# Performance work log

Measured on AMD Instinct MI355X. Metric: run time of the kernel, lower is better.

Reference implementation:

```python
import jax, jax.numpy as jnp
import numpy as np

N_NODES = 50000
N_EDGES = 800000
EDGE_DIM = 16
EMB = 128
BN_EPS = 1e-5


def setup_inputs() -> dict:
    key = jax.random.key(0)
    ks = jax.random.split(key, 8)
    node_feats = jax.random.normal(ks[0], (N_NODES, EMB), jnp.float32)
    edge_feats = jax.random.normal(ks[1], (N_EDGES, EDGE_DIM), jnp.float32)
    src = jax.random.randint(ks[2], (N_EDGES,), 0, N_NODES, dtype=jnp.int32)
    dst = jax.random.randint(ks[3], (N_EDGES,), 0, N_NODES, dtype=jnp.int32)
    def kaiming(k, shape, fan_in):
        return (jax.random.normal(k, shape, jnp.float32) / np.float32(np.sqrt(fan_in)))
    W_edge = kaiming(ks[4], (EDGE_DIM, EMB), EDGE_DIM)
    b_edge = jnp.zeros((EMB,), jnp.float32)
    W1 = kaiming(ks[5], (EMB, 2 * EMB), EMB)
    b1 = jnp.zeros((2 * EMB,), jnp.float32)
    W2 = kaiming(ks[6], (2 * EMB, EMB), 2 * EMB)
    b2 = jnp.zeros((EMB,), jnp.float32)
    bn_gamma = jnp.ones((EMB,), jnp.float32)
    bn_beta = jnp.zeros((EMB,), jnp.float32)
    return dict(node_feats=node_feats, edge_feats=edge_feats, W_edge=W_edge,
                b_edge=b_edge, W1=W1, b1=b1, W2=W2, b2=b2,
                bn_gamma=bn_gamma, bn_beta=bn_beta, src=src, dst=dst)


def reference(node_feats, edge_feats, W_edge, b_edge, W1, b1, W2, b2,
              bn_gamma, bn_beta, src, dst):
    n_nodes = node_feats.shape[0]
    # edge embedding: Linear(num_edge_emb -> emb_dim)
    edge_embeds = edge_feats @ W_edge + b_edge            # [E, D]
    # u_add_e message: gather source node feats, add edge embeds
    msg = node_feats[src] + edge_embeds                   # [E, D]
    # sum aggregation to destination nodes
    agg = jax.ops.segment_sum(msg, dst, num_segments=n_nodes)  # [N, D]
    # MLP: Linear(D, 2D) -> ReLU -> Linear(2D, D)
    h = jax.nn.relu(agg @ W1 + b1) @ W2 + b2              # [N, D]
    # BatchNorm1d over the node (batch) dim, training-mode batch stats
    mean = jnp.mean(h, axis=0)
    var = jnp.mean((h - mean) ** 2, axis=0)               # biased variance
    out = (h - mean) * jax.lax.rsqrt(var + BN_EPS) * bn_gamma + bn_beta
    return out
```

## Files before the change

kernel.cpp:

```cpp
#include <hip/hip_runtime.h>
#include <stdint.h>

#define NN 50000
#define NE 800000
#define CAP 128
#define NB_MLP ((NN + 63) / 64)

typedef unsigned int u32;
typedef unsigned short u16;
typedef __attribute__((ext_vector_type(8))) short short8;
typedef __attribute__((ext_vector_type(4))) float f32x4;
typedef int int4u __attribute__((ext_vector_type(4), aligned(4)));

__device__ __align__(16) u16   g_nf16[NN * 128];
__device__ __align__(16) u16   g_agg16[NN * 128];
__device__ __align__(16) float g_h[NN * 128];
__device__ __align__(16) float g_We[16 * 128];
__device__ __align__(16) float g_be[128];
__device__ __align__(16) float g_b1[256];
__device__ __align__(16) float g_b2[128];
__device__ __align__(16) float g_gamma[128];
__device__ __align__(16) float g_beta[128];
__device__ __align__(16) u16   g_W1p[128 * 256];
__device__ __align__(16) u16   g_W2p[256 * 128];
__device__ __align__(16) int2  g_bkt[NN * CAP];

__device__ __align__(16) int   g_zero[NN + 256];
#define g_cursor (g_zero)
#define g_stats  ((float*)(g_zero + NN))

__device__ __forceinline__ float bf2f(u16 u) {
  return __uint_as_float(((u32)u) << 16);
}
__device__ __forceinline__ u16 f2bf(float x) {
  u32 u = __float_as_uint(x);
  u32 r = (u + 0x7fffu + ((u >> 16) & 1u)) >> 16;
  return (u16)r;
}
__device__ __forceinline__ bool is_bf16(const u32* probe) {
  return probe[0] == 0x3F803F80u;
}

__global__ void k_prep(const void* nodep,
                       const void* We, const void* be, const void* W1,
                       const void* b1, const void* W2, const void* b2,
                       const void* ga, const void* bt, const u32* probe) {
  const bool b16 = is_bf16(probe);
  const int gid = blockIdx.x * blockDim.x + threadIdx.x;
  const int stride = gridDim.x * blockDim.x;
  if (!b16) {
    const float2* s = (const float2*)nodep;
    u32* d = (u32*)g_nf16;
    for (int i = gid; i < NN * 64; i += stride) {
      float2 v = s[i];
      d[i] = (u32)f2bf(v.x) | ((u32)f2bf(v.y) << 16);
    }
  }
  const int i = gid;
  if (i < 2816) {
    const void* s; float* d; int off;
    if      (i < 2048) { s = We; d = g_We;    off = i; }
    else if (i < 2176) { s = be; d = g_be;    off = i - 2048; }
    else if (i < 2432) { s = b1; d = g_b1;    off = i - 2176; }
    else if (i < 2560) { s = b2; d = g_b2;    off = i - 2432; }
    else if (i < 2688) { s = ga; d = g_gamma; off = i - 2560; }
    else               { s = bt; d = g_beta;  off = i - 2688; }
    d[off] = b16 ? bf2f(((const u16*)s)[off]) : ((const float*)s)[off];
  } else if (i < 35584) {
    const int idx = i - 2816;
    const int j = idx & 7, lane = (idx >> 3) & 63, nt = (idx >> 9) & 15, kt = idx >> 13;
    const int k = kt * 32 + (lane >> 4) * 8 + j;
    const int n = nt * 16 + (lane & 15);
    g_W1p[idx] = b16 ? ((const u16*)W1)[k * 256 + n]
                     : f2bf(((const float*)W1)[k * 256 + n]);
  } else if (i < 68352) {
    const int idx = i - 35584;
    const int j = idx & 7, lane = (idx >> 3) & 63, nt = (idx >> 9) & 7, kt = idx >> 12;
    const int k = kt * 32 + (lane >> 4) * 8 + j;
    const int n = nt * 16 + (lane & 15);
    g_W2p[idx] = b16 ? ((const u16*)W2)[k * 128 + n]
                     : f2bf(((const float*)W2)[k * 128 + n]);
  }
}

__global__ __launch_bounds__(256) void scatter_kernel(const int* __restrict__ src,
                                                      const int* __restrict__ dst, int E) {
  const int e = blockIdx.x * blockDim.x + threadIdx.x;
  if (e >= E) return;
  const int d = dst[e];
  const int c = atomicAdd(&g_cursor[d], 1);
  if (c < CAP) g_bkt[d * CAP + c] = make_int2(e, src[e]);
}

__device__ __forceinline__ void accum8(float* acc, uint4 v) {
  const u32 vv[4] = {v.x, v.y, v.z, v.w};
#pragma unroll
  for (int q = 0; q < 4; ++q) {
    acc[2 * q]     += bf2f((u16)vv[q]);
    acc[2 * q + 1] += bf2f((u16)(vv[q] >> 16));
  }
}
template <bool B16>
__device__ __forceinline__ float ef_at(const void* efin, size_t idx) {
  if constexpr (B16) return bf2f(((const u16*)efin)[idx]);
  else               return ((const float*)efin)[idx];
}
template <bool B16>
__device__ __forceinline__ void agg_body(const u16* __restrict__ nf,
                                         const void* __restrict__ efin) {
  const int tid  = threadIdx.x;
  const int wv   = tid >> 6;
  const int lane = tid & 63;
  const int g    = lane >> 4;
  const int i16  = lane & 15;
  const int t    = blockIdx.x * 4 + wv;
  if (t >= NN) return;
  const int degc = g_cursor[t];
  const int deg  = degc < CAP ? degc : CAP;
  const int base = t * CAP;
  const int d0 = i16 * 8;

  const int q4 = deg >> 2, r4 = deg & 3;
  const int gs = g * q4 + (g < r4 ? g : r4);
  const int ge = gs + q4 + (g < r4 ? 1 : 0);

  float acc[8];
#pragma unroll
  for (int q = 0; q < 8; ++q) acc[q] = 0.f;
  float sEF = 0.f;

  int jj = gs;
  for (; jj + 3 < ge; jj += 4) {
    const int* ep = (const int*)g_bkt + 2 * (base + jj);
    int4u ea = *(const int4u*)ep;
    int4u eb = *(const int4u*)(ep + 4);
    uint4 v0 = *(const uint4*)(nf + (size_t)ea.y * 128 + d0);
    uint4 v1 = *(const uint4*)(nf + (size_t)ea.w * 128 + d0);
    uint4 v2 = *(const uint4*)(nf + (size_t)eb.y * 128 + d0);
    uint4 v3 = *(const uint4*)(nf + (size_t)eb.w * 128 + d0);
    float f0 = ef_at<B16>(efin, (size_t)ea.x * 16 + i16);
    float f1 = ef_at<B16>(efin, (size_t)ea.z * 16 + i16);
    float f2 = ef_at<B16>(efin, (size_t)eb.x * 16 + i16);
    float f3 = ef_at<B16>(efin, (size_t)eb.z * 16 + i16);
    accum8(acc, v0);
    accum8(acc, v1);
    accum8(acc, v2);
    accum8(acc, v3);
    sEF += (f0 + f1) + (f2 + f3);
  }
  const int rem = ge - jj;
  if (rem > 0) {
    int2 p0 = g_bkt[base + jj];
    int2 p1 = (rem > 1) ? g_bkt[base + jj + 1] : p0;
    int2 p2 = (rem > 2) ? g_bkt[base + jj + 2] : p0;
    uint4 v0 = *(const uint4*)(nf + (size_t)p0.y * 128 + d0);
    uint4 v1 = *(const uint4*)(nf + (size_t)p1.y * 128 + d0);
    uint4 v2 = *(const uint4*)(nf + (size_t)p2.y * 128 + d0);
    float f0 = ef_at<B16>(efin, (size_t)p0.x * 16 + i16);
    float f1 = ef_at<B16>(efin, (size_t)p1.x * 16 + i16);
    float f2 = ef_at<B16>(efin, (size_t)p2.x * 16 + i16);
    accum8(acc, v0);
    sEF += f0;
    if (rem > 1) { accum8(acc, v1); sEF += f1; }
    if (rem > 2) { accum8(acc, v2); sEF += f2; }
  }

  sEF += __shfl_xor(sEF, 16, 64);
  sEF += __shfl_xor(sEF, 32, 64);

#pragma unroll
  for (int kk = 0; kk < 4; ++kk) {
    const int k = g * 4 + kk;
    const float ek = __shfl(sEF, k, 16);
#pragma unroll
    for (int q = 0; q < 8; ++q)
      acc[q] = fmaf(ek, g_We[k * 128 + d0 + q], acc[q]);
  }
  if (g == 0) {
    const float degf = (float)degc;
#pragma unroll
    for (int q = 0; q < 8; ++q)
      acc[q] = fmaf(degf, g_be[d0 + q], acc[q]);
  }

#pragma unroll
  for (int q = 0; q < 8; ++q) {
    acc[q] += __shfl_xor(acc[q], 16, 64);
    acc[q] += __shfl_xor(acc[q], 32, 64);
  }

  if (g == 0) {
    uint4 o;
    o.x = (u32)f2bf(acc[0]) | ((u32)f2bf(acc[1]) << 16);
    o.y = (u32)f2bf(acc[2]) | ((u32)f2bf(acc[3]) << 16);
    o.z = (u32)f2bf(acc[4]) | ((u32)f2bf(acc[5]) << 16);
    o.w = (u32)f2bf(acc[6]) | ((u32)f2bf(acc[7]) << 16);
    *(uint4*)(g_agg16 + (size_t)t * 128 + d0) = o;
  }
}
__global__ __launch_bounds__(256) void agg_kernel(const void* nfin, const void* efin,
                                                  const u32* probe) {
  if (is_bf16(probe)) agg_body<true>((const u16*)nfin, efin);
  else                agg_body<false>(g_nf16, efin);
}

__global__ __launch_bounds__(256, 4) void mlp_mfma(int N) {
  __shared__ u16 sT[2 * 64 * 136];
  __shared__ float sb1[256];
  __shared__ float sb2[128];
  __shared__ float sStat[256];

  const int tid  = threadIdx.x;
  const int w    = tid >> 6;
  const int lane = tid & 63;
  const int quad = lane >> 4;
  const int l15  = lane & 15;
  const int row0 = blockIdx.x * 64;

  sb1[tid] = g_b1[tid];
  if (tid < 128) sb2[tid] = g_b2[tid];
  sStat[tid] = 0.f;

#pragma unroll
  for (int i = 0; i < 4; ++i) {
    int lin = i * 256 + tid;
    int r = lin >> 4, seg = lin & 15;
    uint4 v = make_uint4(0u, 0u, 0u, 0u);
    if (row0 + r < N)
      v = *(const uint4*)(g_agg16 + ((size_t)(row0 + r) * 128 + seg * 8));
    *(uint4*)(sT + r * 136 + seg * 8) = v;
  }
  __syncthreads();

  f32x4 acc[2][4];

#pragma unroll
  for (int p = 0; p < 2; ++p) {
    const int ntb = (p == 0) ? (8 + 2 * w) : (2 * w);
#pragma unroll
    for (int nti = 0; nti < 2; ++nti)
#pragma unroll
      for (int m = 0; m < 4; ++m)
        acc[nti][m] = (f32x4){0.f, 0.f, 0.f, 0.f};
#pragma unroll
    for (int kt = 0; kt < 4; ++kt) {
      short8 a[4];
#pragma unroll
      for (int m = 0; m < 4; ++m)
        a[m] = *(const short8*)(sT + (m * 16 + l15) * 136 + kt * 32 + quad * 8);
#pragma unroll
      for (int nti = 0; nti < 2; ++nti) {
        short8 b = *(const short8*)(g_W1p + ((kt * 16 + ntb + nti) * 64 + lane) * 8);
#pragma unroll
        for (int m = 0; m < 4; ++m)
          acc[nti][m] = __builtin_amdgcn_mfma_f32_16x16x32_bf16(a[m], b, acc[nti][m], 0, 0, 0);
      }
    }
    if (p == 1) __syncthreads();
    u16* dstT = (p == 0) ? (sT + 8704) : sT;
    const int cb = (p == 0) ? (ntb - 8) * 16 : ntb * 16;
#pragma unroll
    for (int nti = 0; nti < 2; ++nti) {
      float bias = sb1[(ntb + nti) * 16 + l15];
#pragma unroll
      for (int m = 0; m < 4; ++m)
#pragma unroll
        for (int reg = 0; reg < 4; ++reg) {
          float v = acc[nti][m][reg] + bias;
          v = v > 0.f ? v : 0.f;
          dstT[(m * 16 + quad * 4 + reg) * 136 + cb + nti * 16 + l15] = f2bf(v);
        }
    }
  }
  __syncthreads();

#pragma unroll
  for (int nti = 0; nti < 2; ++nti)
#pragma unroll
    for (int m = 0; m < 4; ++m)
      acc[nti][m] = (f32x4){0.f, 0.f, 0.f, 0.f};
#pragma unroll
  for (int kt = 0; kt < 8; ++kt) {
    const u16* srcT = (kt < 4) ? sT : (sT + 8704);
    const int kc = (kt & 3) * 32 + quad * 8;
    short8 a[4];
#pragma unroll
    for (int m = 0; m < 4; ++m)
      a[m] = *(const short8*)(srcT + (m * 16 + l15) * 136 + kc);
#pragma unroll
    for (int nti = 0; nti < 2; ++nti) {
      short8 b = *(const short8*)(g_W2p + ((kt * 8 + 2 * w + nti) * 64 + lane) * 8);
#pragma unroll
      for (int m = 0; m < 4; ++m)
        acc[nti][m] = __builtin_amdgcn_mfma_f32_16x16x32_bf16(a[m], b, acc[nti][m], 0, 0, 0);
    }
  }

#pragma unroll
  for (int nti = 0; nti < 2; ++nti) {
    const int col = (2 * w + nti) * 16 + l15;
    const float bias = sb2[col];
    float ss = 0.f, sq = 0.f;
#pragma unroll
    for (int m = 0; m < 4; ++m)
#pragma unroll
      for (int reg = 0; reg < 4; ++reg) {
        const int row = row0 + m * 16 + quad * 4 + reg;
        if (row < N) {
          float hv = acc[nti][m][reg] + bias;
          g_h[(size_t)row * 128 + col] = hv;
          ss += hv;
          sq += hv * hv;
        }
      }
    atomicAdd(&sStat[col], ss);
    atomicAdd(&sStat[128 + col], sq);
  }
  __syncthreads();
  atomicAdd(&g_stats[tid], sStat[tid]);
}

__global__ void bn_kernel(const u32* probe, void* outp, int N) {
  const bool b16 = is_bf16(probe);
  const float invN = 1.0f / (float)N;
  int i = blockIdx.x * blockDim.x + threadIdx.x;
  const int total = N * 32;
  const int stride = gridDim.x * blockDim.x;
  for (; i < total; i += stride) {
    int c4 = (i & 31) * 4;
    float4 hv = ((const float4*)g_h)[i];
    float in[4] = {hv.x, hv.y, hv.z, hv.w};
    float o[4];
#pragma unroll
    for (int j = 0; j < 4; ++j) {
      int c = c4 + j;
      float mean = g_stats[c] * invN;
      float var  = g_stats[128 + c] * invN - mean * mean;
      float sc   = rsqrtf(var + 1e-5f) * g_gamma[c];
      o[j] = (in[j] - mean) * sc + g_beta[c];
    }
    if (b16) {
      ((ushort4*)outp)[i] = make_ushort4(f2bf(o[0]), f2bf(o[1]), f2bf(o[2]), f2bf(o[3]));
    } else {
      ((float4*)outp)[i] = make_float4(o[0], o[1], o[2], o[3]);
    }
  }
}

extern "C" void kernel_launch(void* const* d_in, const int* in_sizes, int n_in,
                              void* d_out, int out_size, void* d_ws, size_t ws_size,
                              hipStream_t stream) {
  const int N = in_sizes[0] / 128;
  const int E = in_sizes[10];
  const u32* probe = (const u32*)d_in[8];
  const int* src = (const int*)d_in[10];
  const int* dst = (const int*)d_in[11];

  static void* zp = nullptr;
  if (!zp) hipGetSymbolAddress(&zp, HIP_SYMBOL(g_zero));
  hipMemsetAsync(zp, 0, (NN + 256) * sizeof(int), stream);

  hipLaunchKernelGGL(k_prep, dim3(1024), dim3(256), 0, stream,
                     d_in[0], d_in[2], d_in[3], d_in[4], d_in[5],
                     d_in[6], d_in[7], d_in[8], d_in[9], probe);
  const int ebl = (E + 255) / 256;
  hipLaunchKernelGGL(scatter_kernel, dim3(ebl), dim3(256), 0, stream, src, dst, E);
  hipLaunchKernelGGL(agg_kernel, dim3((NN + 3) / 4), dim3(256), 0, stream,
                     d_in[0], d_in[1], probe);
  hipLaunchKernelGGL(mlp_mfma, dim3(NB_MLP), dim3(256), 0, stream, N);
  hipLaunchKernelGGL(bn_kernel, dim3(2048), dim3(256), 0, stream,
                     probe, d_out, N);
}
```

Before: 293.3 us.

## Fuse edge scatter into prep kernel and use one 16-lane group per node

```diff
diff --git a/kernel.cpp b/kernel.cpp
--- a/kernel.cpp
+++ b/kernel.cpp
@@ -3,7 +3,7 @@
 
 #define NN 50000
 #define NE 800000
-#define CAP 128
+#define CAP 64
 #define NB_MLP ((NN + 63) / 64)
 
 typedef unsigned int u32;
@@ -41,13 +41,19 @@
   return probe[0] == 0x3F803F80u;
 }
 
-__global__ void k_prep(const void* nodep,
+__global__ void k_prep(const int* __restrict__ src, const int* __restrict__ dst,
+                       int E, const void* nodep,
                        const void* We, const void* be, const void* W1,
                        const void* b1, const void* W2, const void* b2,
                        const void* ga, const void* bt, const u32* probe) {
   const bool b16 = is_bf16(probe);
   const int gid = blockIdx.x * blockDim.x + threadIdx.x;
   const int stride = gridDim.x * blockDim.x;
+  for (int e = gid; e < E; e += stride) {
+    const int d = dst[e];
+    const int c = atomicAdd(&g_cursor[d], 1);
+    if (c < CAP) g_bkt[d * CAP + c] = make_int2(e, src[e]);
+  }
   if (!b16) {
     const float2* s = (const float2*)nodep;
     u32* d = (u32*)g_nf16;
@@ -83,15 +89,6 @@
   }
 }
 
-__global__ __launch_bounds__(256) void scatter_kernel(const int* __restrict__ src,
-                                                      const int* __restrict__ dst, int E) {
-  const int e = blockIdx.x * blockDim.x + threadIdx.x;
-  if (e >= E) return;
-  const int d = dst[e];
-  const int c = atomicAdd(&g_cursor[d], 1);
-  if (c < CAP) g_bkt[d * CAP + c] = make_int2(e, src[e]);
-}
-
 __device__ __forceinline__ void accum8(float* acc, uint4 v) {
   const u32 vv[4] = {v.x, v.y, v.z, v.w};
 #pragma unroll
@@ -109,28 +106,54 @@
 __device__ __forceinline__ void agg_body(const u16* __restrict__ nf,
                                          const void* __restrict__ efin) {
   const int tid  = threadIdx.x;
-  const int wv   = tid >> 6;
-  const int lane = tid & 63;
-  const int g    = lane >> 4;
-  const int i16  = lane & 15;
-  const int t    = blockIdx.x * 4 + wv;
+  const int i16  = tid & 15;
+  const int grp  = tid >> 4;
+  const int t    = blockIdx.x * 16 + grp;
   if (t >= NN) return;
   const int degc = g_cursor[t];
   const int deg  = degc < CAP ? degc : CAP;
   const int base = t * CAP;
-  const int d0 = i16 * 8;
-
-  const int q4 = deg >> 2, r4 = deg & 3;
-  const int gs = g * q4 + (g < r4 ? g : r4);
-  const int ge = gs + q4 + (g < r4 ? 1 : 0);
+  const int d0   = i16 * 8;
 
   float acc[8];
 #pragma unroll
   for (int q = 0; q < 8; ++q) acc[q] = 0.f;
   float sEF = 0.f;
 
-  int jj = gs;
-  for (; jj + 3 < ge; jj += 4) {
+  int jj = 0;
+  for (; jj + 7 < deg; jj += 8) {
+    const int* ep = (const int*)g_bkt + 2 * (base + jj);
+    int4u ea = *(const int4u*)ep;
+    int4u eb = *(const int4u*)(ep + 4);
+    int4u ec = *(const int4u*)(ep + 8);
+    int4u ed = *(const int4u*)(ep + 12);
+    uint4 v0 = *(const uint4*)(nf + (size_t)ea.y * 128 + d0);
+    uint4 v1 = *(const uint4*)(nf + (size_t)ea.w * 128 + d0);
+    uint4 v2 = *(const uint4*)(nf + (size_t)eb.y * 128 + d0);
+    uint4 v3 = *(const uint4*)(nf + (size_t)eb.w * 128 + d0);
+    uint4 v4 = *(const uint4*)(nf + (size_t)ec.y * 128 + d0);
+    uint4 v5 = *(const uint4*)(nf + (size_t)ec.w * 128 + d0);
+    uint4 v6 = *(const uint4*)(nf + (size_t)ed.y * 128 + d0);
+    uint4 v7 = *(const uint4*)(nf + (size_t)ed.w * 128 + d0);
+    float f0 = ef_at<B16>(efin, (size_t)ea.x * 16 + i16);
+    float f1 = ef_at<B16>(efin, (size_t)ea.z * 16 + i16);
+    float f2 = ef_at<B16>(efin, (size_t)eb.x * 16 + i16);
+    float f3 = ef_at<B16>(efin, (size_t)eb.z * 16 + i16);
+    float f4 = ef_at<B16>(efin, (size_t)ec.x * 16 + i16);
+    float f5 = ef_at<B16>(efin, (size_t)ec.z * 16 + i16);
+    float f6 = ef_at<B16>(efin, (size_t)ed.x * 16 + i16);
+    float f7 = ef_at<B16>(efin, (size_t)ed.z * 16 + i16);
+    accum8(acc, v0);
+    accum8(acc, v1);
+    accum8(acc, v2);
+    accum8(acc, v3);
+    accum8(acc, v4);
+    accum8(acc, v5);
+    accum8(acc, v6);
+    accum8(acc, v7);
+    sEF += ((f0 + f1) + (f2 + f3)) + ((f4 + f5) + (f6 + f7));
+  }
+  for (; jj + 3 < deg; jj += 4) {
     const int* ep = (const int*)g_bkt + 2 * (base + jj);
     int4u ea = *(const int4u*)ep;
     int4u eb = *(const int4u*)(ep + 4);
@@ -148,7 +171,7 @@
     accum8(acc, v3);
     sEF += (f0 + f1) + (f2 + f3);
   }
-  const int rem = ge - jj;
+  const int rem = deg - jj;
   if (rem > 0) {
     int2 p0 = g_bkt[base + jj];
     int2 p1 = (rem > 1) ? g_bkt[base + jj + 1] : p0;
@@ -165,38 +188,24 @@
     if (rem > 2) { accum8(acc, v2); sEF += f2; }
   }
 
-  sEF += __shfl_xor(sEF, 16, 64);
-  sEF += __shfl_xor(sEF, 32, 64);
-
-#pragma unroll
-  for (int kk = 0; kk < 4; ++kk) {
-    const int k = g * 4 + kk;
+#pragma unroll
+  for (int k = 0; k < 16; ++k) {
     const float ek = __shfl(sEF, k, 16);
 #pragma unroll
     for (int q = 0; q < 8; ++q)
       acc[q] = fmaf(ek, g_We[k * 128 + d0 + q], acc[q]);
   }
-  if (g == 0) {
-    const float degf = (float)degc;
-#pragma unroll
-    for (int q = 0; q < 8; ++q)
-      acc[q] = fmaf(degf, g_be[d0 + q], acc[q]);
-  }
-
-#pragma unroll
-  for (int q = 0; q < 8; ++q) {
-    acc[q] += __shfl_xor(acc[q], 16, 64);
-    acc[q] += __shfl_xor(acc[q], 32, 64);
-  }
-
-  if (g == 0) {
-    uint4 o;
-    o.x = (u32)f2bf(acc[0]) | ((u32)f2bf(acc[1]) << 16);
-    o.y = (u32)f2bf(acc[2]) | ((u32)f2bf(acc[3]) << 16);
-    o.z = (u32)f2bf(acc[4]) | ((u32)f2bf(acc[5]) << 16);
-    o.w = (u32)f2bf(acc[6]) | ((u32)f2bf(acc[7]) << 16);
-    *(uint4*)(g_agg16 + (size_t)t * 128 + d0) = o;
-  }
+  const float degf = (float)degc;
+#pragma unroll
+  for (int q = 0; q < 8; ++q)
+    acc[q] = fmaf(degf, g_be[d0 + q], acc[q]);
+
+  uint4 o;
+  o.x = (u32)f2bf(acc[0]) | ((u32)f2bf(acc[1]) << 16);
+  o.y = (u32)f2bf(acc[2]) | ((u32)f2bf(acc[3]) << 16);
+  o.z = (u32)f2bf(acc[4]) | ((u32)f2bf(acc[5]) << 16);
+  o.w = (u32)f2bf(acc[6]) | ((u32)f2bf(acc[7]) << 16);
+  *(uint4*)(g_agg16 + (size_t)t * 128 + d0) = o;
 }
 __global__ __launch_bounds__(256) void agg_kernel(const void* nfin, const void* efin,
                                                   const u32* probe) {
@@ -360,12 +369,10 @@
   if (!zp) hipGetSymbolAddress(&zp, HIP_SYMBOL(g_zero));
   hipMemsetAsync(zp, 0, (NN + 256) * sizeof(int), stream);
 
-  hipLaunchKernelGGL(k_prep, dim3(1024), dim3(256), 0, stream,
-                     d_in[0], d_in[2], d_in[3], d_in[4], d_in[5],
+  hipLaunchKernelGGL(k_prep, dim3(2048), dim3(256), 0, stream,
+                     src, dst, E, d_in[0], d_in[2], d_in[3], d_in[4], d_in[5],
                      d_in[6], d_in[7], d_in[8], d_in[9], probe);
-  const int ebl = (E + 255) / 256;
-  hipLaunchKernelGGL(scatter_kernel, dim3(ebl), dim3(256), 0, stream, src, dst, E);
-  hipLaunchKernelGGL(agg_kernel, dim3((NN + 3) / 4), dim3(256), 0, stream,
+  hipLaunchKernelGGL(agg_kernel, dim3((NN + 15) / 16), dim3(256), 0, stream,
                      d_in[0], d_in[1], probe);
   hipLaunchKernelGGL(mlp_mfma, dim3(NB_MLP), dim3(256), 0, stream, N);
   hipLaunchKernelGGL(bn_kernel, dim3(2048), dim3(256), 0, stream,
```

Result: no change. 288.5 us (-1.6%).

## Fuse scatter into prep and store edge features inline in 64-byte buckets

Applied to the files above, without the earlier changes.

```diff
diff --git a/kernel.cpp b/kernel.cpp
--- a/kernel.cpp
+++ b/kernel.cpp
@@ -3,14 +3,13 @@
 
 #define NN 50000
 #define NE 800000
-#define CAP 128
+#define CAP 64
 #define NB_MLP ((NN + 63) / 64)
 
 typedef unsigned int u32;
 typedef unsigned short u16;
 typedef __attribute__((ext_vector_type(8))) short short8;
 typedef __attribute__((ext_vector_type(4))) float f32x4;
-typedef int int4u __attribute__((ext_vector_type(4), aligned(4)));
 
 __device__ __align__(16) u16   g_nf16[NN * 128];
 __device__ __align__(16) u16   g_agg16[NN * 128];
@@ -23,7 +22,7 @@
 __device__ __align__(16) float g_beta[128];
 __device__ __align__(16) u16   g_W1p[128 * 256];
 __device__ __align__(16) u16   g_W2p[256 * 128];
-__device__ __align__(16) int2  g_bkt[NN * CAP];
+__device__ __align__(64) u32   g_bkt[(size_t)NN * CAP * 16];
 
 __device__ __align__(16) int   g_zero[NN + 256];
 #define g_cursor (g_zero)
@@ -37,23 +36,52 @@
   u32 r = (u + 0x7fffu + ((u >> 16) & 1u)) >> 16;
   return (u16)r;
 }
+__device__ __forceinline__ u32 f2bf2(float lo, float hi) {
+  return (u32)f2bf(lo) | ((u32)f2bf(hi) << 16);
+}
 __device__ __forceinline__ bool is_bf16(const u32* probe) {
   return probe[0] == 0x3F803F80u;
 }
 
-__global__ void k_prep(const void* nodep,
+__global__ void k_prep(const int* __restrict__ src, const int* __restrict__ dst,
+                       int E, const void* nodep, const void* efp,
                        const void* We, const void* be, const void* W1,
                        const void* b1, const void* W2, const void* b2,
                        const void* ga, const void* bt, const u32* probe) {
   const bool b16 = is_bf16(probe);
   const int gid = blockIdx.x * blockDim.x + threadIdx.x;
   const int stride = gridDim.x * blockDim.x;
+  for (int e = gid; e < E; e += stride) {
+    const int d = dst[e];
+    const int c = atomicAdd(&g_cursor[d], 1);
+    if (c < CAP) {
+      u32* p = g_bkt + ((size_t)d * CAP + c) * 16;
+      u32 w1, w2, w3, w4, w5, w6, w7, w8;
+      if (b16) {
+        const uint4* s4 = (const uint4*)efp + (size_t)e * 2;
+        uint4 a = s4[0], b = s4[1];
+        w1 = a.x; w2 = a.y; w3 = a.z; w4 = a.w;
+        w5 = b.x; w6 = b.y; w7 = b.z; w8 = b.w;
+      } else {
+        const float4* s4 = (const float4*)efp + (size_t)e * 4;
+        float4 a = s4[0], b = s4[1], c2 = s4[2], d2 = s4[3];
+        w1 = f2bf2(a.x, a.y);  w2 = f2bf2(a.z, a.w);
+        w3 = f2bf2(b.x, b.y);  w4 = f2bf2(b.z, b.w);
+        w5 = f2bf2(c2.x, c2.y); w6 = f2bf2(c2.z, c2.w);
+        w7 = f2bf2(d2.x, d2.y); w8 = f2bf2(d2.z, d2.w);
+      }
+      *(uint4*)p        = make_uint4((u32)src[e], w1, w2, w3);
+      *(uint4*)(p + 4)  = make_uint4(w4, w5, w6, w7);
+      *(uint4*)(p + 8)  = make_uint4(w8, 0u, 0u, 0u);
+      *(uint4*)(p + 12) = make_uint4(0u, 0u, 0u, 0u);
+    }
+  }
   if (!b16) {
     const float2* s = (const float2*)nodep;
     u32* d = (u32*)g_nf16;
     for (int i = gid; i < NN * 64; i += stride) {
       float2 v = s[i];
-      d[i] = (u32)f2bf(v.x) | ((u32)f2bf(v.y) << 16);
+      d[i] = f2bf2(v.x, v.y);
     }
   }
   const int i = gid;
@@ -83,15 +111,6 @@
   }
 }
 
-__global__ __launch_bounds__(256) void scatter_kernel(const int* __restrict__ src,
-                                                      const int* __restrict__ dst, int E) {
-  const int e = blockIdx.x * blockDim.x + threadIdx.x;
-  if (e >= E) return;
-  const int d = dst[e];
-  const int c = atomicAdd(&g_cursor[d], 1);
-  if (c < CAP) g_bkt[d * CAP + c] = make_int2(e, src[e]);
-}
-
 __device__ __forceinline__ void accum8(float* acc, uint4 v) {
   const u32 vv[4] = {v.x, v.y, v.z, v.w};
 #pragma unroll
@@ -100,14 +119,8 @@
     acc[2 * q + 1] += bf2f((u16)(vv[q] >> 16));
   }
 }
-template <bool B16>
-__device__ __forceinline__ float ef_at(const void* efin, size_t idx) {
-  if constexpr (B16) return bf2f(((const u16*)efin)[idx]);
-  else               return ((const float*)efin)[idx];
-}
-template <bool B16>
-__device__ __forceinline__ void agg_body(const u16* __restrict__ nf,
-                                         const void* __restrict__ efin) {
+__global__ __launch_bounds__(256) void agg_kernel(const void* nfin, const u32* probe) {
+  const u16* __restrict__ nf = is_bf16(probe) ? (const u16*)nfin : g_nf16;
   const int tid  = threadIdx.x;
   const int wv   = tid >> 6;
   const int lane = tid & 63;
@@ -117,7 +130,7 @@
   if (t >= NN) return;
   const int degc = g_cursor[t];
   const int deg  = degc < CAP ? degc : CAP;
-  const int base = t * CAP;
+  const size_t base = (size_t)t * CAP;
   const int d0 = i16 * 8;
 
   const int q4 = deg >> 2, r4 = deg & 3;
@@ -131,17 +144,19 @@
 
   int jj = gs;
   for (; jj + 3 < ge; jj += 4) {
-    const int* ep = (const int*)g_bkt + 2 * (base + jj);
-    int4u ea = *(const int4u*)ep;
-    int4u eb = *(const int4u*)(ep + 4);
-    uint4 v0 = *(const uint4*)(nf + (size_t)ea.y * 128 + d0);
-    uint4 v1 = *(const uint4*)(nf + (size_t)ea.w * 128 + d0);
-    uint4 v2 = *(const uint4*)(nf + (size_t)eb.y * 128 + d0);
-    uint4 v3 = *(const uint4*)(nf + (size_t)eb.w * 128 + d0);
-    float f0 = ef_at<B16>(efin, (size_t)ea.x * 16 + i16);
-    float f1 = ef_at<B16>(efin, (size_t)ea.z * 16 + i16);
-    float f2 = ef_at<B16>(efin, (size_t)eb.x * 16 + i16);
-    float f3 = ef_at<B16>(efin, (size_t)eb.z * 16 + i16);
+    const u32* p0 = g_bkt + (base + jj) * 16;
+    const u32* p1 = p0 + 16;
+    const u32* p2 = p0 + 32;
+    const u32* p3 = p0 + 48;
+    u32 s0 = p0[0], s1 = p1[0], s2 = p2[0], s3 = p3[0];
+    float f0 = bf2f(((const u16*)p0)[2 + i16]);
+    float f1 = bf2f(((const u16*)p1)[2 + i16]);
+    float f2 = bf2f(((const u16*)p2)[2 + i16]);
+    float f3 = bf2f(((const u16*)p3)[2 + i16]);
+    uint4 v0 = *(const uint4*)(nf + (size_t)s0 * 128 + d0);
+    uint4 v1 = *(const uint4*)(nf + (size_t)s1 * 128 + d0);
+    uint4 v2 = *(const uint4*)(nf + (size_t)s2 * 128 + d0);
+    uint4 v3 = *(const uint4*)(nf + (size_t)s3 * 128 + d0);
     accum8(acc, v0);
     accum8(acc, v1);
     accum8(acc, v2);
@@ -150,15 +165,16 @@
   }
   const int rem = ge - jj;
   if (rem > 0) {
-    int2 p0 = g_bkt[base + jj];
-    int2 p1 = (rem > 1) ? g_bkt[base + jj + 1] : p0;
-    int2 p2 = (rem > 2) ? g_bkt[base + jj + 2] : p0;
-    uint4 v0 = *(const uint4*)(nf + (size_t)p0.y * 128 + d0);
-    uint4 v1 = *(const uint4*)(nf + (size_t)p1.y * 128 + d0);
-    uint4 v2 = *(const uint4*)(nf + (size_t)p2.y * 128 + d0);
-    float f0 = ef_at<B16>(efin, (size_t)p0.x * 16 + i16);
-    float f1 = ef_at<B16>(efin, (size_t)p1.x * 16 + i16);
-    float f2 = ef_at<B16>(efin, (size_t)p2.x * 16 + i16);
+    const u32* p0 = g_bkt + (base + jj) * 16;
+    const u32* p1 = (rem > 1) ? p0 + 16 : p0;
+    const u32* p2 = (rem > 2) ? p0 + 32 : p0;
+    u32 s0 = p0[0], s1 = p1[0], s2 = p2[0];
+    float f0 = bf2f(((const u16*)p0)[2 + i16]);
+    float f1 = bf2f(((const u16*)p1)[2 + i16]);
+    float f2 = bf2f(((const u16*)p2)[2 + i16]);
+    uint4 v0 = *(const uint4*)(nf + (size_t)s0 * 128 + d0);
+    uint4 v1 = *(const uint4*)(nf + (size_t)s1 * 128 + d0);
+    uint4 v2 = *(const uint4*)(nf + (size_t)s2 * 128 + d0);
     accum8(acc, v0);
     sEF += f0;
     if (rem > 1) { accum8(acc, v1); sEF += f1; }
@@ -191,17 +207,12 @@
 
   if (g == 0) {
     uint4 o;
-    o.x = (u32)f2bf(acc[0]) | ((u32)f2bf(acc[1]) << 16);
-    o.y = (u32)f2bf(acc[2]) | ((u32)f2bf(acc[3]) << 16);
-    o.z = (u32)f2bf(acc[4]) | ((u32)f2bf(acc[5]) << 16);
-    o.w = (u32)f2bf(acc[6]) | ((u32)f2bf(acc[7]) << 16);
+    o.x = f2bf2(acc[0], acc[1]);
+    o.y = f2bf2(acc[2], acc[3]);
+    o.z = f2bf2(acc[4], acc[5]);
+    o.w = f2bf2(acc[6], acc[7]);
     *(uint4*)(g_agg16 + (size_t)t * 128 + d0) = o;
   }
-}
-__global__ __launch_bounds__(256) void agg_kernel(const void* nfin, const void* efin,
-                                                  const u32* probe) {
-  if (is_bf16(probe)) agg_body<true>((const u16*)nfin, efin);
-  else                agg_body<false>(g_nf16, efin);
 }
 
 __global__ __launch_bounds__(256, 4) void mlp_mfma(int N) {
@@ -307,7 +318,7 @@
       for (int reg = 0; reg < 4; ++reg) {
         const int row = row0 + m * 16 + quad * 4 + reg;
         if (row < N) {
-          float hv = acc[nti][m][reg] + bias;
+          const float hv = acc[nti][m][reg] + bias;
           g_h[(size_t)row * 128 + col] = hv;
           ss += hv;
           sq += hv * hv;
@@ -360,13 +371,11 @@
   if (!zp) hipGetSymbolAddress(&zp, HIP_SYMBOL(g_zero));
   hipMemsetAsync(zp, 0, (NN + 256) * sizeof(int), stream);
 
-  hipLaunchKernelGGL(k_prep, dim3(1024), dim3(256), 0, stream,
-                     d_in[0], d_in[2], d_in[3], d_in[4], d_in[5],
-                     d_in[6], d_in[7], d_in[8], d_in[9], probe);
-  const int ebl = (E + 255) / 256;
-  hipLaunchKernelGGL(scatter_kernel, dim3(ebl), dim3(256), 0, stream, src, dst, E);
+  hipLaunchKernelGGL(k_prep, dim3(2048), dim3(256), 0, stream,
+                     src, dst, E, d_in[0], d_in[1], d_in[2], d_in[3], d_in[4],
+                     d_in[5], d_in[6], d_in[7], d_in[8], d_in[9], probe);
   hipLaunchKernelGGL(agg_kernel, dim3((NN + 3) / 4), dim3(256), 0, stream,
-                     d_in[0], d_in[1], probe);
+                     d_in[0], probe);
   hipLaunchKernelGGL(mlp_mfma, dim3(NB_MLP), dim3(256), 0, stream, N);
   hipLaunchKernelGGL(bn_kernel, dim3(2048), dim3(256), 0, stream,
                      probe, d_out, N);
```

Result: faster. 285.5 us (-2.7%).
